# Kernel optimization log

Hardware: AMD Instinct MI355X
Metric: run time of the kernel (lower is better)

The kernel has to match this reference:

```python
import jax, jax.numpy as jnp
import numpy as np

EMBED_DIM = 1024
NUM_HEADS = 16
HEAD_DIM = 64


def setup_inputs() -> dict:
    key = jax.random.key(0)
    k_x, k_wqkv, k_bqkv, k_wo, k_bo = jax.random.split(key, 5)
    hd = NUM_HEADS * HEAD_DIM
    x = jax.random.normal(k_x, (2, 2048, EMBED_DIM), dtype=jnp.float32)
    # nn.Linear-style init scale
    s1 = 1.0 / np.sqrt(EMBED_DIM)
    s2 = 1.0 / np.sqrt(hd)
    W_qkv = jax.random.uniform(k_wqkv, (EMBED_DIM, 3 * hd), jnp.float32, -s1, s1)
    b_qkv = jax.random.uniform(k_bqkv, (3 * hd,), jnp.float32, -s1, s1)
    W_out = jax.random.uniform(k_wo, (hd, EMBED_DIM), jnp.float32, -s2, s2)
    b_out = jax.random.uniform(k_bo, (EMBED_DIM,), jnp.float32, -s2, s2)
    return {"x": x, "W_qkv": W_qkv, "b_qkv": b_qkv, "W_out": W_out, "b_out": b_out}


def reference(x, W_qkv, b_qkv, W_out, b_out):
    b, s, _ = x.shape
    h, d = NUM_HEADS, HEAD_DIM
    qkv = x @ W_qkv + b_qkv                      # [b, s, 3*h*d]
    qkv = qkv.reshape(b, s, 3, h, d)             # packed order (three, h, d)
    q, k, v = qkv[:, :, 0], qkv[:, :, 1], qkv[:, :, 2]  # each [b, s, h, d]
    scale = 1.0 / jnp.sqrt(jnp.asarray(d, x.dtype))
    scores = jnp.einsum('bshd,bthd->bhst', q, k) * scale  # [b, h, s, s]
    probs = jax.nn.softmax(scores, axis=-1)
    out = jnp.einsum('bhst,bthd->bshd', probs, v)          # [b, s, h, d]
    out = out.reshape(b, s, h * d)
    return out @ W_out + b_out                   # [b, s, embed_dim]
```

## Files before the change

kernel.cpp:

```cpp
#include <hip/hip_runtime.h>

typedef __attribute__((ext_vector_type(8))) short short8;
typedef __attribute__((ext_vector_type(4))) float f32x4;
typedef unsigned short u16;
typedef unsigned int u32;
typedef unsigned long long u64;

#define EMBED 1024
#define SEQ 2048
#define NH 16
#define HD 64

#define MFMA(a, b, c) __builtin_amdgcn_mfma_f32_16x16x32_bf16(a, b, c, 0, 0, 0)

__device__ __forceinline__ u16 f2bf(float f) {
  union { float f; u32 u; } v; v.f = f;
  u32 r = v.u + 0x7fffu + ((v.u >> 16) & 1u);
  return (u16)(r >> 16);
}

__device__ __forceinline__ u32 cvtpk(float lo, float hi) {
  u32 r;
  asm("v_cvt_pk_bf16_f32 %0, %1, %2" : "=v"(r) : "v"(lo), "v"(hi));
  return r;
}

__device__ __forceinline__ float ex2(float x) { return __builtin_amdgcn_exp2f(x); }

__device__ __forceinline__ void async16(const void* g, void* l) {
  __builtin_amdgcn_global_load_lds(
      (const __attribute__((address_space(1))) void*)(uintptr_t)g,
      (__attribute__((address_space(3))) void*)(u32)(uintptr_t)l, 16, 0, 0);
}

__global__ __launch_bounds__(256) void prep_kernel(
    const float* __restrict__ x, u16* __restrict__ xb,
    const float* __restrict__ Wq, u16* __restrict__ Wqt,
    const float* __restrict__ Wo, u16* __restrict__ Wot) {
  int bx = blockIdx.x;
  if (bx < 4096) {
    int i = bx * 256 + threadIdx.x;
    float4 v = ((const float4*)x)[i];
    u64 pk = (u64)f2bf(v.x) | ((u64)f2bf(v.y) << 16) | ((u64)f2bf(v.z) << 32) |
             ((u64)f2bf(v.w) << 48);
    ((u64*)xb)[i] = pk;
    return;
  }
  __shared__ float tile[32][33];
  const int K = 1024;
  int bx2 = bx - 4096;
  int nb = bx2 & 127, kb = bx2 >> 7;
  const float* W; u16* Wt; int N, n0;
  if (nb < 96) { W = Wq; Wt = Wqt; N = 3072; n0 = nb * 32; }
  else         { W = Wo; Wt = Wot; N = 1024; n0 = (nb - 96) * 32; }
  int k0 = kb * 32;
  int tx = threadIdx.x & 31, ty = threadIdx.x >> 5;
#pragma unroll
  for (int p = 0; p < 4; ++p)
    tile[ty + 8 * p][tx] = W[(u64)(k0 + ty + 8 * p) * N + n0 + tx];
  __syncthreads();
#pragma unroll
  for (int p = 0; p < 4; ++p)
    Wt[(u64)(n0 + ty + 8 * p) * K + k0 + tx] = f2bf(tile[tx][ty + 8 * p]);
}

__global__ __launch_bounds__(256) void gemm_qkv_kernel(
    const u16* __restrict__ A, const u16* __restrict__ Bt, const float* __restrict__ bias,
    u16* __restrict__ qb, u16* __restrict__ kb, u16* __restrict__ vtb) {
  __shared__ u16 As[2][128 * 32];
  __shared__ u16 Bs[2][128 * 32];
  const int K = 1024;
  int m0 = blockIdx.y * 128, n0 = blockIdx.x * 128;
  int tid = threadIdx.x, w = tid >> 6, lane = tid & 63;
  int wm = w >> 1, wn = w & 1;
  int c = lane & 15, g = lane >> 4;

  f32x4 acc[4][4] = {};

  int srow = lane >> 2;
  int scol = (lane & 3) * 8;
  const u16* a0 = A + (u64)m0 * K;
  const u16* b0 = Bt + (u64)n0 * K;

  auto stage = [&](int buf, int kt) {
#pragma unroll
    for (int i = 0; i < 2; ++i) {
      int chunk = w * 2 + i;
      int row = chunk * 16 + srow;
      async16(a0 + (u64)row * K + kt + scol, (char*)As[buf] + chunk * 1024 + lane * 16);
      async16(b0 + (u64)row * K + kt + scol, (char*)Bs[buf] + chunk * 1024 + lane * 16);
    }
  };

  auto body = [&](int cur, int kt, bool last) {
    if (!last) {
      stage(cur ^ 1, kt + 32);
      asm volatile("s_waitcnt vmcnt(4)" ::: "memory");
    } else {
      asm volatile("s_waitcnt vmcnt(0)" ::: "memory");
    }
    __builtin_amdgcn_s_barrier();
    asm volatile("" ::: "memory");
    short8 af[4], bfr[4];
#pragma unroll
    for (int i = 0; i < 4; ++i)
      af[i] = *(const short8*)(As[cur] + (wm * 64 + i * 16 + c) * 32 + g * 8);
#pragma unroll
    for (int j = 0; j < 4; ++j)
      bfr[j] = *(const short8*)(Bs[cur] + (wn * 64 + j * 16 + c) * 32 + g * 8);
#pragma unroll
    for (int i = 0; i < 4; ++i)
#pragma unroll
      for (int j = 0; j < 4; ++j)
        acc[i][j] = MFMA(af[i], bfr[j], acc[i][j]);
    asm volatile("s_waitcnt lgkmcnt(0)" ::: "memory");
    __builtin_amdgcn_s_barrier();
    asm volatile("" ::: "memory");
  };

  stage(0, 0);
  for (int kt = 0; kt < K; kt += 64) {
    body(0, kt, false);
    body(1, kt + 32, kt + 64 >= K);
  }

  const float QSCALE = 0.125f * 1.44269504f;
#pragma unroll
  for (int j = 0; j < 4; ++j) {
    int col = n0 + wn * 64 + j * 16 + c;
    float bv = bias[col];
    int sel = col >> 10;
    int h = (col & 1023) >> 6, d = col & 63;
#pragma unroll
    for (int i = 0; i < 4; ++i) {
      int rowb = m0 + wm * 64 + i * 16 + g * 4;
      int b = rowb >> 11, s = rowb & 2047;
      int bh = b * NH + h;
      if (sel == 0) {
#pragma unroll
        for (int r = 0; r < 4; ++r)
          qb[((u64)bh * SEQ + (s + r)) * HD + d] = f2bf((acc[i][j][r] + bv) * QSCALE);
      } else if (sel == 1) {
#pragma unroll
        for (int r = 0; r < 4; ++r)
          kb[((u64)bh * SEQ + (s + r)) * HD + d] = f2bf(acc[i][j][r] + bv);
      } else {
        u64 pk = 0;
#pragma unroll
        for (int r = 0; r < 4; ++r) pk |= (u64)f2bf(acc[i][j][r] + bv) << (16 * r);
        *(u64*)(vtb + ((u64)bh * HD + d) * SEQ + s) = pk;
      }
    }
  }
}

__global__ __launch_bounds__(256, 4) void attn_kernel(const u16* __restrict__ qb,
                                                      const u16* __restrict__ kb,
                                                      const u16* __restrict__ vtb,
                                                      u16* __restrict__ aout) {
  __shared__ __align__(16) u16 Ks[2][64 * 64];
  __shared__ __align__(16) u16 Vts[2][64 * 64];
  __shared__ __align__(16) u16 Pb[4][16 * 64];
  int bh = blockIdx.y;
  int q0 = blockIdx.x * 64;
  int tid = threadIdx.x, w = tid >> 6, lane = tid & 63;
  int c = lane & 15, g = lane >> 4;

  const u16* Qb = qb + ((u64)bh * SEQ + q0 + w * 16) * HD;
  short8 qf[2];
#pragma unroll
  for (int ks = 0; ks < 2; ++ks)
    qf[ks] = *(const short8*)(Qb + c * HD + ks * 32 + g * 8);

  f32x4 o[4] = {};
  f32x4 lacc = {};

  int sr = lane >> 3;
  int se = 8 * ((lane & 7) ^ sr);
  char* Pw = (char*)&Pb[w][0] + c * 128;
  u32 pswz = (c & 7) << 4;
  const u16* kbase = kb + (u64)bh * SEQ * HD;
  const u16* vbase = vtb + (u64)bh * HD * SEQ;

  auto stage = [&](int buf, int t0) {
#pragma unroll
    for (int i = 0; i < 2; ++i) {
      int chunk = w * 2 + i;
      int row = chunk * 8 + sr;
      async16(kbase + (u64)(t0 + row) * HD + se,
              (char*)Ks[buf] + chunk * 1024 + lane * 16);
      async16(vbase + (u64)row * SEQ + t0 + se,
              (char*)Vts[buf] + chunk * 1024 + lane * 16);
    }
  };

  auto body = [&](int cur, int t0, bool last) {
    if (!last) {
      stage(cur ^ 1, t0 + 64);
      asm volatile("s_waitcnt vmcnt(4)" ::: "memory");
    } else {
      asm volatile("s_waitcnt vmcnt(0)" ::: "memory");
    }
    __builtin_amdgcn_s_barrier();
    asm volatile("" ::: "memory");

    const u16* KsC = Ks[cur];
    const u16* VtsC = Vts[cur];

    f32x4 s[4] = {};
    __builtin_amdgcn_s_setprio(1);
#pragma unroll
    for (int j = 0; j < 4; ++j) {
      int trow = j * 16 + c;
      int sw = (trow & 7) << 4;
#pragma unroll
      for (int ks = 0; ks < 2; ++ks) {
        short8 ak = *(const short8*)((const char*)KsC + trow * 128 +
                                     ((g * 16 + ks * 64) ^ sw));
        s[j] = MFMA(ak, qf[ks], s[j]);
      }
    }
    __builtin_amdgcn_s_setprio(0);

    f32x4 p0, p1, p2, p3;
#pragma unroll
    for (int r = 0; r < 4; ++r) {
      p0[r] = ex2(s[0][r]);
      p1[r] = ex2(s[1][r]);
      p2[r] = ex2(s[2][r]);
      p3[r] = ex2(s[3][r]);
    }
    lacc += (p0 + p1) + (p2 + p3);

    {
      u64 w0 = (u64)cvtpk(p0[0], p0[1]) | ((u64)cvtpk(p0[2], p0[3]) << 32);
      u64 w1 = (u64)cvtpk(p1[0], p1[1]) | ((u64)cvtpk(p1[2], p1[3]) << 32);
      u64 w2 = (u64)cvtpk(p2[0], p2[1]) | ((u64)cvtpk(p2[2], p2[3]) << 32);
      u64 w3 = (u64)cvtpk(p3[0], p3[1]) | ((u64)cvtpk(p3[2], p3[3]) << 32);
      *(u64*)(Pw + ((g * 8 + 0)  ^ pswz)) = w0;
      *(u64*)(Pw + ((g * 8 + 32) ^ pswz)) = w1;
      *(u64*)(Pw + ((g * 8 + 64) ^ pswz)) = w2;
      *(u64*)(Pw + ((g * 8 + 96) ^ pswz)) = w3;
    }

    __builtin_amdgcn_s_setprio(1);
#pragma unroll
    for (int ks = 0; ks < 2; ++ks) {
      short8 pa = *(const short8*)(Pw + ((ks * 64 + g * 16) ^ pswz));
#pragma unroll
      for (int jd = 0; jd < 4; ++jd) {
        int drow = jd * 16 + c;
        int sw = (drow & 7) << 4;
        short8 bv = *(const short8*)((const char*)VtsC + drow * 128 +
                                     ((g * 16 + ks * 64) ^ sw));
        o[jd] = MFMA(pa, bv, o[jd]);
      }
    }
    __builtin_amdgcn_s_setprio(0);

    asm volatile("s_waitcnt lgkmcnt(0)" ::: "memory");
    __builtin_amdgcn_s_barrier();
    asm volatile("" ::: "memory");
  };

  stage(0, 0);
  const int NT = SEQ / 64;
  for (int it = 0; it < NT; it += 2) {
    body(0, it * 64, false);
    body(1, it * 64 + 64, it + 2 >= NT);
  }

  float l = (lacc[0] + lacc[1]) + (lacc[2] + lacc[3]);
  l += __shfl_xor(l, 16);
  l += __shfl_xor(l, 32);
  float inv = 1.0f / l;
  float invr[4];
#pragma unroll
  for (int r = 0; r < 4; ++r) invr[r] = __shfl(inv, g * 4 + r);
  int hh = bh & 15, b = bh >> 4;
#pragma unroll
  for (int r = 0; r < 4; ++r) {
    int q = q0 + w * 16 + g * 4 + r;
#pragma unroll
    for (int jd = 0; jd < 4; ++jd)
      aout[(u64)(b * SEQ + q) * EMBED + hh * HD + jd * 16 + c] =
          f2bf(o[jd][r] * invr[r]);
  }
}

__global__ __launch_bounds__(256) void gemm_out_kernel(const u16* __restrict__ A,
                                                       const u16* __restrict__ Bt,
                                                       const float* __restrict__ bias,
                                                       float* __restrict__ out) {
  __shared__ u16 As[2][128 * 32];
  __shared__ u16 Bs[2][64 * 32];
  const int K = 1024;
  int m0 = blockIdx.y * 128, n0 = blockIdx.x * 64;
  int tid = threadIdx.x, w = tid >> 6, lane = tid & 63;
  int wm = w >> 1, wn = w & 1;
  int c = lane & 15, g = lane >> 4;

  f32x4 acc[4][2] = {};
  int srow = lane >> 2;
  int scol = (lane & 3) * 8;
  const u16* a0 = A + (u64)m0 * K;
  const u16* b0 = Bt + (u64)n0 * K;

  auto stage = [&](int buf, int kt) {
#pragma unroll
    for (int i = 0; i < 2; ++i) {
      int chunk = w * 2 + i;
      int row = chunk * 16 + srow;
      async16(a0 + (u64)row * K + kt + scol, (char*)As[buf] + chunk * 1024 + lane * 16);
    }
    int brow = w * 16 + srow;
    async16(b0 + (u64)brow * K + kt + scol, (char*)Bs[buf] + w * 1024 + lane * 16);
  };

  auto body = [&](int cur, int kt, bool last) {
    if (!last) {
      stage(cur ^ 1, kt + 32);
      asm volatile("s_waitcnt vmcnt(3)" ::: "memory");
    } else {
      asm volatile("s_waitcnt vmcnt(0)" ::: "memory");
    }
    __builtin_amdgcn_s_barrier();
    asm volatile("" ::: "memory");
    short8 af[4], bfr[2];
#pragma unroll
    for (int i = 0; i < 4; ++i)
      af[i] = *(const short8*)(As[cur] + (wm * 64 + i * 16 + c) * 32 + g * 8);
#pragma unroll
    for (int j = 0; j < 2; ++j)
      bfr[j] = *(const short8*)(Bs[cur] + (wn * 32 + j * 16 + c) * 32 + g * 8);
#pragma unroll
    for (int i = 0; i < 4; ++i)
#pragma unroll
      for (int j = 0; j < 2; ++j)
        acc[i][j] = MFMA(af[i], bfr[j], acc[i][j]);
    asm volatile("s_waitcnt lgkmcnt(0)" ::: "memory");
    __builtin_amdgcn_s_barrier();
    asm volatile("" ::: "memory");
  };

  stage(0, 0);
  for (int kt = 0; kt < K; kt += 64) {
    body(0, kt, false);
    body(1, kt + 32, kt + 64 >= K);
  }

#pragma unroll
  for (int j = 0; j < 2; ++j) {
    int col = n0 + wn * 32 + j * 16 + c;
    float bv = bias[col];
#pragma unroll
    for (int i = 0; i < 4; ++i) {
      int rowb = m0 + wm * 64 + i * 16 + g * 4;
#pragma unroll
      for (int r = 0; r < 4; ++r)
        out[(u64)(rowb + r) * EMBED + col] = acc[i][j][r] + bv;
    }
  }
}

extern "C" void kernel_launch(void* const* d_in, const int* in_sizes, int n_in,
                              void* d_out, int out_size, void* d_ws, size_t ws_size,
                              hipStream_t stream) {
  const float* x = (const float*)d_in[0];
  const float* Wqkv = (const float*)d_in[1];
  const float* bqkv = (const float*)d_in[2];
  const float* Wout = (const float*)d_in[3];
  const float* bout = (const float*)d_in[4];
  float* out = (float*)d_out;
  char* ws = (char*)d_ws;

  u16* xb  = (u16*)(ws);
  u16* wqt = (u16*)(ws + (8ull << 20));
  u16* wot = (u16*)(ws + (14ull << 20));
  u16* qb  = (u16*)(ws + (16ull << 20));
  u16* kb  = (u16*)(ws + (24ull << 20));
  u16* vtb = (u16*)(ws + (32ull << 20));
  u16* aout = xb;

  prep_kernel<<<dim3(8192), dim3(256), 0, stream>>>(x, xb, Wqkv, wqt, Wout, wot);
  gemm_qkv_kernel<<<dim3(24, 32), dim3(256), 0, stream>>>(xb, wqt, bqkv, qb, kb, vtb);
  attn_kernel<<<dim3(32, 32), dim3(256), 0, stream>>>(qb, kb, vtb, aout);
  gemm_out_kernel<<<dim3(16, 32), dim3(256), 0, stream>>>(aout, wot, bout, out);
}
```

Measured before the change: 120.4 us.

## Process two query sub-tiles per wave in attention and remap block order

Each wave now handles 32 query rows instead of 16, so every K and V^T fragment read from LDS feeds two MFMAs. This halves K/V staging and LDS reads per query. Each block therefore covers 128 queries, the grid shrinks to 512 blocks, and the launch bound drops to 2 blocks per CU to make room for the extra registers. The 1D block index is also remapped so that consecutive blocks land on different heads, which likely targets L2/XCD locality. The cost is lower occupancy and fewer blocks to fill the CUs.

```diff
diff --git a/kernel.cpp b/kernel.cpp
--- a/kernel.cpp
+++ b/kernel.cpp
@@ -154,26 +154,30 @@
   }
 }
 
-__global__ __launch_bounds__(256, 4) void attn_kernel(const u16* __restrict__ qb,
+__global__ __launch_bounds__(256, 2) void attn_kernel(const u16* __restrict__ qb,
                                                       const u16* __restrict__ kb,
                                                       const u16* __restrict__ vtb,
                                                       u16* __restrict__ aout) {
   __shared__ __align__(16) u16 Ks[2][64 * 64];
   __shared__ __align__(16) u16 Vts[2][64 * 64];
-  __shared__ __align__(16) u16 Pb[4][16 * 64];
-  int bh = blockIdx.y;
-  int q0 = blockIdx.x * 64;
+  __shared__ __align__(16) u16 Pb[4][32 * 64];
+  int bid = blockIdx.x;
+  int wg = (bid & 7) * 64 + (bid >> 3);
+  int bh = wg >> 4;
+  int q0 = (wg & 15) * 128;
   int tid = threadIdx.x, w = tid >> 6, lane = tid & 63;
   int c = lane & 15, g = lane >> 4;
 
-  const u16* Qb = qb + ((u64)bh * SEQ + q0 + w * 16) * HD;
-  short8 qf[2];
-#pragma unroll
-  for (int ks = 0; ks < 2; ++ks)
-    qf[ks] = *(const short8*)(Qb + c * HD + ks * 32 + g * 8);
-
-  f32x4 o[4] = {};
-  f32x4 lacc = {};
+  const u16* Qb = qb + ((u64)bh * SEQ + q0 + w * 32) * HD;
+  short8 qf[2][2];
+#pragma unroll
+  for (int i = 0; i < 2; ++i)
+#pragma unroll
+    for (int ks = 0; ks < 2; ++ks)
+      qf[i][ks] = *(const short8*)(Qb + (i * 16 + c) * HD + ks * 32 + g * 8);
+
+  f32x4 o[2][4] = {};
+  f32x4 lacc[2] = {};
 
   int sr = lane >> 3;
   int se = 8 * ((lane & 7) ^ sr);
@@ -207,7 +211,7 @@
     const u16* KsC = Ks[cur];
     const u16* VtsC = Vts[cur];
 
-    f32x4 s[4] = {};
+    f32x4 s0[4] = {}, s1[4] = {};
     __builtin_amdgcn_s_setprio(1);
 #pragma unroll
     for (int j = 0; j < 4; ++j) {
@@ -217,43 +221,54 @@
       for (int ks = 0; ks < 2; ++ks) {
         short8 ak = *(const short8*)((const char*)KsC + trow * 128 +
                                      ((g * 16 + ks * 64) ^ sw));
-        s[j] = MFMA(ak, qf[ks], s[j]);
+        s0[j] = MFMA(ak, qf[0][ks], s0[j]);
+        s1[j] = MFMA(ak, qf[1][ks], s1[j]);
       }
     }
     __builtin_amdgcn_s_setprio(0);
 
-    f32x4 p0, p1, p2, p3;
-#pragma unroll
-    for (int r = 0; r < 4; ++r) {
-      p0[r] = ex2(s[0][r]);
-      p1[r] = ex2(s[1][r]);
-      p2[r] = ex2(s[2][r]);
-      p3[r] = ex2(s[3][r]);
-    }
-    lacc += (p0 + p1) + (p2 + p3);
+#pragma unroll
+    for (int j = 0; j < 4; ++j)
+#pragma unroll
+      for (int r = 0; r < 4; ++r) {
+        s0[j][r] = ex2(s0[j][r]);
+        s1[j][r] = ex2(s1[j][r]);
+      }
+    lacc[0] += (s0[0] + s0[1]) + (s0[2] + s0[3]);
+    lacc[1] += (s1[0] + s1[1]) + (s1[2] + s1[3]);
 
     {
-      u64 w0 = (u64)cvtpk(p0[0], p0[1]) | ((u64)cvtpk(p0[2], p0[3]) << 32);
-      u64 w1 = (u64)cvtpk(p1[0], p1[1]) | ((u64)cvtpk(p1[2], p1[3]) << 32);
-      u64 w2 = (u64)cvtpk(p2[0], p2[1]) | ((u64)cvtpk(p2[2], p2[3]) << 32);
-      u64 w3 = (u64)cvtpk(p3[0], p3[1]) | ((u64)cvtpk(p3[2], p3[3]) << 32);
-      *(u64*)(Pw + ((g * 8 + 0)  ^ pswz)) = w0;
-      *(u64*)(Pw + ((g * 8 + 32) ^ pswz)) = w1;
-      *(u64*)(Pw + ((g * 8 + 64) ^ pswz)) = w2;
-      *(u64*)(Pw + ((g * 8 + 96) ^ pswz)) = w3;
+      u64 a0 = (u64)cvtpk(s0[0][0], s0[0][1]) | ((u64)cvtpk(s0[0][2], s0[0][3]) << 32);
+      u64 a1 = (u64)cvtpk(s0[1][0], s0[1][1]) | ((u64)cvtpk(s0[1][2], s0[1][3]) << 32);
+      u64 a2 = (u64)cvtpk(s0[2][0], s0[2][1]) | ((u64)cvtpk(s0[2][2], s0[2][3]) << 32);
+      u64 a3 = (u64)cvtpk(s0[3][0], s0[3][1]) | ((u64)cvtpk(s0[3][2], s0[3][3]) << 32);
+      *(u64*)(Pw + ((g * 8 + 0)  ^ pswz)) = a0;
+      *(u64*)(Pw + ((g * 8 + 32) ^ pswz)) = a1;
+      *(u64*)(Pw + ((g * 8 + 64) ^ pswz)) = a2;
+      *(u64*)(Pw + ((g * 8 + 96) ^ pswz)) = a3;
+      u64 b0 = (u64)cvtpk(s1[0][0], s1[0][1]) | ((u64)cvtpk(s1[0][2], s1[0][3]) << 32);
+      u64 b1 = (u64)cvtpk(s1[1][0], s1[1][1]) | ((u64)cvtpk(s1[1][2], s1[1][3]) << 32);
+      u64 b2 = (u64)cvtpk(s1[2][0], s1[2][1]) | ((u64)cvtpk(s1[2][2], s1[2][3]) << 32);
+      u64 b3 = (u64)cvtpk(s1[3][0], s1[3][1]) | ((u64)cvtpk(s1[3][2], s1[3][3]) << 32);
+      *(u64*)(Pw + 2048 + ((g * 8 + 0)  ^ pswz)) = b0;
+      *(u64*)(Pw + 2048 + ((g * 8 + 32) ^ pswz)) = b1;
+      *(u64*)(Pw + 2048 + ((g * 8 + 64) ^ pswz)) = b2;
+      *(u64*)(Pw + 2048 + ((g * 8 + 96) ^ pswz)) = b3;
     }
 
     __builtin_amdgcn_s_setprio(1);
 #pragma unroll
     for (int ks = 0; ks < 2; ++ks) {
-      short8 pa = *(const short8*)(Pw + ((ks * 64 + g * 16) ^ pswz));
+      short8 pa0 = *(const short8*)(Pw + ((ks * 64 + g * 16) ^ pswz));
+      short8 pa1 = *(const short8*)(Pw + 2048 + ((ks * 64 + g * 16) ^ pswz));
 #pragma unroll
       for (int jd = 0; jd < 4; ++jd) {
         int drow = jd * 16 + c;
         int sw = (drow & 7) << 4;
         short8 bv = *(const short8*)((const char*)VtsC + drow * 128 +
                                      ((g * 16 + ks * 64) ^ sw));
-        o[jd] = MFMA(pa, bv, o[jd]);
+        o[0][jd] = MFMA(pa0, bv, o[0][jd]);
+        o[1][jd] = MFMA(pa1, bv, o[1][jd]);
       }
     }
     __builtin_amdgcn_s_setprio(0);
@@ -270,21 +285,24 @@
     body(1, it * 64 + 64, it + 2 >= NT);
   }
 
-  float l = (lacc[0] + lacc[1]) + (lacc[2] + lacc[3]);
-  l += __shfl_xor(l, 16);
-  l += __shfl_xor(l, 32);
-  float inv = 1.0f / l;
-  float invr[4];
-#pragma unroll
-  for (int r = 0; r < 4; ++r) invr[r] = __shfl(inv, g * 4 + r);
   int hh = bh & 15, b = bh >> 4;
 #pragma unroll
-  for (int r = 0; r < 4; ++r) {
-    int q = q0 + w * 16 + g * 4 + r;
-#pragma unroll
-    for (int jd = 0; jd < 4; ++jd)
-      aout[(u64)(b * SEQ + q) * EMBED + hh * HD + jd * 16 + c] =
-          f2bf(o[jd][r] * invr[r]);
+  for (int i = 0; i < 2; ++i) {
+    float l = (lacc[i][0] + lacc[i][1]) + (lacc[i][2] + lacc[i][3]);
+    l += __shfl_xor(l, 16);
+    l += __shfl_xor(l, 32);
+    float inv = 1.0f / l;
+    float invr[4];
+#pragma unroll
+    for (int r = 0; r < 4; ++r) invr[r] = __shfl(inv, g * 4 + r);
+#pragma unroll
+    for (int r = 0; r < 4; ++r) {
+      int q = q0 + w * 32 + i * 16 + g * 4 + r;
+#pragma unroll
+      for (int jd = 0; jd < 4; ++jd)
+        aout[(u64)(b * SEQ + q) * EMBED + hh * HD + jd * 16 + c] =
+            f2bf(o[i][jd][r] * invr[r]);
+    }
   }
 }
 
@@ -384,6 +402,6 @@
 
   prep_kernel<<<dim3(8192), dim3(256), 0, stream>>>(x, xb, Wqkv, wqt, Wout, wot);
   gemm_qkv_kernel<<<dim3(24, 32), dim3(256), 0, stream>>>(xb, wqt, bqkv, qb, kb, vtb);
-  attn_kernel<<<dim3(32, 32), dim3(256), 0, stream>>>(qb, kb, vtb, aout);
+  attn_kernel<<<dim3(512), dim3(256), 0, stream>>>(qb, kb, vtb, aout);
   gemm_out_kernel<<<dim3(16, 32), dim3(256), 0, stream>>>(aout, wot, bout, out);
 }
```

Result: faster. 116.2 us (-3.5%).
